# Optimization experiments

Hardware: AMD Instinct MI355X
Metric: run time of the kernel (lower is better)

## Reference

```python
import jax, jax.numpy as jnp
import numpy as np

DIM = 1024
HEADS = 16
HEAD_DIM = DIM // HEADS
SCALE = HEAD_DIM ** -0.5


def setup_inputs() -> dict:
    key = jax.random.key(0)
    k_x, k_qkv, k_ow, k_ob = jax.random.split(key, 4)
    B, N = 4, 2048
    x = jax.random.normal(k_x, (B, N, DIM), dtype=jnp.float32)
    # nn.Linear(dim, 3*dim, bias=False): weight [3*dim, dim]; we store transposed [dim, 3*dim]
    w_qkv = jax.random.normal(k_qkv, (DIM, 3 * DIM), dtype=jnp.float32) * (DIM ** -0.5)
    w_out = jax.random.normal(k_ow, (DIM, DIM), dtype=jnp.float32) * (DIM ** -0.5)
    b_out = jax.random.normal(k_ob, (DIM,), dtype=jnp.float32) * 0.01
    return {"x": x, "w_qkv": w_qkv, "w_out": w_out, "b_out": b_out}


def reference(x, w_qkv, w_out, b_out):
    B, N, D = x.shape
    H, hd = HEADS, HEAD_DIM
    qkv = x @ w_qkv                                  # [B, N, 3D]
    qkv = qkv.reshape(B, N, 3, H, hd).transpose(2, 0, 3, 1, 4)  # [3, B, H, N, hd]
    q, k, v = qkv[0], qkv[1], qkv[2]
    dots = jnp.einsum('bhnd,bhmd->bhnm', q, k) * SCALE  # [B, H, N, N]
    attn = jax.nn.softmax(dots, axis=-1)
    out = jnp.einsum('bhnm,bhmd->bhnd', attn, v)     # [B, H, N, hd]
    out = out.transpose(0, 2, 1, 3).reshape(B, N, D)
    return out @ w_out + b_out
```

## Files before the change

kernel.cpp:

```cpp
#include <hip/hip_runtime.h>
#include <hip/hip_bf16.h>

#define BSZ   4
#define NSEQ  2048
#define DIMM  1024
#define NHEAD 16
#define HD    64
#define N3    (3*DIMM)
#define MTOK  (BSZ*NSEQ)
#define SCALE 0.125f
#define CQ    0.18033688011112042f

typedef __attribute__((ext_vector_type(8))) short    short8;
typedef __attribute__((ext_vector_type(4))) short    short4v;
typedef __attribute__((ext_vector_type(2))) unsigned uint2v;
typedef __attribute__((ext_vector_type(8))) __bf16   bf16x8;
typedef __attribute__((ext_vector_type(4))) float    f32x4;

__device__ inline short f2bf(float f) {
    unsigned u = __builtin_bit_cast(unsigned, f);
    u += 0x7fffu + ((u >> 16) & 1u);
    return (short)(u >> 16);
}

__device__ inline unsigned pack_bf16(float a, float b) {
    unsigned ua = __builtin_bit_cast(unsigned, a) + 0x8000u;
    unsigned ub = __builtin_bit_cast(unsigned, b) + 0x8000u;
    return __builtin_amdgcn_perm(ub, ua, 0x07060302u);
}

__device__ inline float fast_exp2(float x) {
#if __has_builtin(__builtin_amdgcn_exp2f)
    return __builtin_amdgcn_exp2f(x);
#else
    return exp2f(x);
#endif
}

__device__ inline bf16x8 lds_frag(const short* p) {
    return __builtin_bit_cast(bf16x8, *(const short8*)p);
}

__device__ inline bf16x8 glb_frag(const short* p) {
    return __builtin_bit_cast(bf16x8, *(const short8*)p);
}

__device__ inline void gld_lds16(const short* g, short* l) {
    __builtin_amdgcn_global_load_lds(
        (const __attribute__((address_space(1))) void*)g,
        (__attribute__((address_space(3))) void*)l, 16, 0, 0);
}

__global__ __launch_bounds__(256)
void cvt_bf16(const float* __restrict__ src, short* __restrict__ dst, int n8)
{
    int i = blockIdx.x * 256 + threadIdx.x;
    if (i >= n8) return;
    float4 v0 = ((const float4*)src)[i * 2];
    float4 v1 = ((const float4*)src)[i * 2 + 1];
    short8 s = { f2bf(v0.x), f2bf(v0.y), f2bf(v0.z), f2bf(v0.w),
                 f2bf(v1.x), f2bf(v1.y), f2bf(v1.z), f2bf(v1.w) };
    ((short8*)dst)[i] = s;
}

__global__ __launch_bounds__(256)
void transpose_bf16(const float* __restrict__ src, short* __restrict__ dst,
                    int K, int N)
{
    __shared__ float tile[32][33];
    const int n0 = blockIdx.x * 32, k0 = blockIdx.y * 32;
    const int tx = threadIdx.x, ty = threadIdx.y;
    #pragma unroll
    for (int i = 0; i < 4; ++i)
        tile[ty + i * 8][tx] = src[(size_t)(k0 + ty + i * 8) * N + n0 + tx];
    __syncthreads();
    #pragma unroll
    for (int i = 0; i < 4; ++i)
        dst[(size_t)(n0 + ty + i * 8) * K + k0 + tx] = f2bf(tile[tx][ty + i * 8]);
}

#define GEMM_KLOOP(APTR, BPTR)                                                 \
    for (int k0 = 0; k0 < DIMM; k0 += 32) {                                    \
        _Pragma("unroll")                                                      \
        for (int j = 0; j < 2; ++j) {                                          \
            int c = j * 256 + tid;                                             \
            int r = c >> 2, jj = c & 3;                                        \
            int gc = jj ^ ((r >> 1) & 3);                                      \
            gld_lds16(APTR + (size_t)(row0 + r) * DIMM + k0 + gc * 8,          \
                      As + c * 8);                                             \
            gld_lds16(BPTR + (size_t)(col0 + r) * DIMM + k0 + gc * 8,         \
                      Bs + c * 8);                                             \
        }                                                                      \
        __syncthreads();                                                       \
        bf16x8 af[4], bfr[4];                                                  \
        _Pragma("unroll")                                                      \
        for (int mt = 0; mt < 4; ++mt) {                                       \
            int row = wm + mt * 16 + l16;                                      \
            af[mt] = lds_frag(&As[row * 32 + (quad ^ ((row >> 1) & 3)) * 8]);  \
        }                                                                      \
        _Pragma("unroll")                                                      \
        for (int nt = 0; nt < 4; ++nt) {                                       \
            int row = wn + nt * 16 + l16;                                      \
            bfr[nt] = lds_frag(&Bs[row * 32 + (quad ^ ((row >> 1) & 3)) * 8]); \
        }                                                                      \
        _Pragma("unroll")                                                      \
        for (int mt = 0; mt < 4; ++mt)                                         \
            _Pragma("unroll")                                                  \
            for (int nt = 0; nt < 4; ++nt)                                     \
                acc[mt][nt] = __builtin_amdgcn_mfma_f32_16x16x32_bf16(         \
                    af[mt], bfr[nt], acc[mt][nt], 0, 0, 0);                    \
        __syncthreads();                                                       \
    }

__global__ __launch_bounds__(256, 2)
void gemm_qkv(const short* __restrict__ a, const short* __restrict__ bt,
              short* __restrict__ qo, short* __restrict__ ko,
              short* __restrict__ vo)
{
    __shared__ short As[128 * 32];
    __shared__ short Bs[128 * 32];
    const int tid  = threadIdx.x;
    const int wave = tid >> 6, lane = tid & 63;
    const int quad = lane >> 4, l16 = lane & 15;
    const int row0 = blockIdx.x * 128, col0 = blockIdx.y * 128;
    const int wm = (wave >> 1) * 64, wn = (wave & 1) * 64;

    f32x4 acc[4][4] = {};
    GEMM_KLOOP(a, bt)

    #pragma unroll
    for (int mt = 0; mt < 4; ++mt) {
        #pragma unroll
        for (int nt = 0; nt < 4; ++nt) {
            int gcol  = col0 + wn + nt * 16 + l16;
            int which = gcol >> 10;
            int cc    = gcol & 1023;
            int h     = cc >> 6, d = cc & 63;
            int growb = row0 + wm + mt * 16 + quad * 4;
            int b_    = growb >> 11;
            int n_    = growb & 2047;
            int bh    = b_ * NHEAD + h;
            if (which == 2) {
                short4v s = { f2bf(acc[mt][nt][0]), f2bf(acc[mt][nt][1]),
                              f2bf(acc[mt][nt][2]), f2bf(acc[mt][nt][3]) };
                *(short4v*)(vo + ((size_t)bh * HD + d) * NSEQ + n_) = s;
            } else if (which == 0) {
                #pragma unroll
                for (int r = 0; r < 4; ++r)
                    qo[((size_t)bh * NSEQ + n_ + r) * HD + d] =
                        f2bf(acc[mt][nt][r] * CQ);
            } else {
                #pragma unroll
                for (int r = 0; r < 4; ++r)
                    ko[((size_t)bh * NSEQ + n_ + r) * HD + d] = f2bf(acc[mt][nt][r]);
            }
        }
    }
}

__global__ __launch_bounds__(256, 3)
void attn(const short* __restrict__ q, const short* __restrict__ k,
          const short* __restrict__ vt, short* __restrict__ o)
{
    __shared__ short Ks[2][64 * 64];
    __shared__ short Ps[4][32 * 72];

    const int tid  = threadIdx.x;
    const int wave = tid >> 6, lane = tid & 63;
    const int quad = lane >> 4, l16 = lane & 15;
    const int bh   = blockIdx.y;
    const int q0   = blockIdx.x * 128;
    const size_t qkbase = (size_t)bh * NSEQ * HD;
    const size_t vbase  = (size_t)bh * HD * NSEQ;

    bf16x8 qf[2][2];
    #pragma unroll
    for (int g = 0; g < 2; ++g)
        #pragma unroll
        for (int ks = 0; ks < 2; ++ks)
            qf[g][ks] = glb_frag(q + qkbase +
                (size_t)(q0 + wave * 32 + g * 16 + l16) * HD + ks * 32 + quad * 8);

    f32x4 oacc[4][2] = {};
    float lsum[2] = {0.f, 0.f};
    short* Pw = &Ps[wave][0];

    const int  sr   = tid >> 3, sj = tid & 7;
    const int  soff = sr * HD + ((sj ^ (sr & 7)) * 8);
    const short* kbh = k + qkbase;

    gld_lds16(kbh + soff,            &Ks[0][tid * 8]);
    gld_lds16(kbh + soff + 32 * HD,  &Ks[0][2048 + tid * 8]);

    for (int t = 0; t < NSEQ / 64; ++t) {
        const int kv0 = t * 64;
        __syncthreads();
        if (t + 1 < NSEQ / 64) {
            const short* src = kbh + (size_t)(kv0 + 64) * HD;
            short* dst = &Ks[(t + 1) & 1][0];
            gld_lds16(src + soff,           dst + tid * 8);
            gld_lds16(src + soff + 32 * HD, dst + 2048 + tid * 8);
        }
        const short* Kb = &Ks[t & 1][0];

        bf16x8 vf[2][4];
        #pragma unroll
        for (int ks2 = 0; ks2 < 2; ++ks2)
            #pragma unroll
            for (int ot = 0; ot < 4; ++ot)
                vf[ks2][ot] = glb_frag(vt + vbase +
                    (size_t)(ot * 16 + l16) * NSEQ + kv0 + ks2 * 32 + quad * 8);

        f32x4 sacc[4][2] = {};
        #pragma unroll
        for (int nt = 0; nt < 4; ++nt) {
            int row = nt * 16 + l16;
            #pragma unroll
            for (int ks = 0; ks < 2; ++ks) {
                bf16x8 kf = lds_frag(&Kb[row * 64 + (((ks * 4 + quad) ^ (row & 7)) * 8)]);
                #pragma unroll
                for (int g = 0; g < 2; ++g)
                    sacc[nt][g] = __builtin_amdgcn_mfma_f32_16x16x32_bf16(
                        kf, qf[g][ks], sacc[nt][g], 0, 0, 0);
            }
        }

        #pragma unroll
        for (int g = 0; g < 2; ++g) {
            #pragma unroll
            for (int nt = 0; nt < 4; ++nt) {
                float p0 = fast_exp2(sacc[nt][g][0]);
                float p1 = fast_exp2(sacc[nt][g][1]);
                float p2 = fast_exp2(sacc[nt][g][2]);
                float p3 = fast_exp2(sacc[nt][g][3]);
                lsum[g] += (p0 + p1) + (p2 + p3);
                uint2v u = { pack_bf16(p0, p1), pack_bf16(p2, p3) };
                *(uint2v*)&Pw[(g * 16 + l16) * 72 + nt * 16 + quad * 4] = u;
            }
        }

        #pragma unroll
        for (int ks2 = 0; ks2 < 2; ++ks2) {
            bf16x8 pf[2];
            #pragma unroll
            for (int g = 0; g < 2; ++g)
                pf[g] = lds_frag(&Pw[(g * 16 + l16) * 72 + ks2 * 32 + quad * 8]);
            #pragma unroll
            for (int ot = 0; ot < 4; ++ot)
                #pragma unroll
                for (int g = 0; g < 2; ++g)
                    oacc[ot][g] = __builtin_amdgcn_mfma_f32_16x16x32_bf16(
                        vf[ks2][ot], pf[g], oacc[ot][g], 0, 0, 0);
        }
    }

    const int b_ = bh >> 4, h = bh & 15;
    float inv[2];
    #pragma unroll
    for (int g = 0; g < 2; ++g) {
        float l = lsum[g];
        l += __shfl_xor(l, 16);
        l += __shfl_xor(l, 32);
        inv[g] = 1.f / l;
    }
    #pragma unroll
    for (int ot = 0; ot < 4; ++ot) {
        #pragma unroll
        for (int g = 0; g < 2; ++g) {
            short4v s4 = { f2bf(oacc[ot][g][0] * inv[g]),
                           f2bf(oacc[ot][g][1] * inv[g]),
                           f2bf(oacc[ot][g][2] * inv[g]),
                           f2bf(oacc[ot][g][3] * inv[g]) };
            *(short4v*)(o + ((size_t)b_ * NSEQ + q0 + wave * 32 + g * 16 + l16) * DIMM +
                        h * HD + ot * 16 + quad * 4) = s4;
        }
    }
}

__global__ __launch_bounds__(256, 3)
void gemm_out(const short* __restrict__ a, const short* __restrict__ bt,
              const float* __restrict__ bias, float* __restrict__ out)
{
    __shared__ short As[64 * 32];
    __shared__ short Bs[128 * 32];
    const int tid  = threadIdx.x;
    const int wave = tid >> 6, lane = tid & 63;
    const int quad = lane >> 4, l16 = lane & 15;
    const int row0 = blockIdx.x * 64, col0 = blockIdx.y * 128;
    const int wm = (wave & 1) * 32, wn = (wave >> 1) * 64;

    f32x4 acc[2][4] = {};

    for (int k0 = 0; k0 < DIMM; k0 += 32) {
        {
            int r = tid >> 2, jj = tid & 3;
            int gc = jj ^ ((r >> 1) & 3);
            gld_lds16(a + (size_t)(row0 + r) * DIMM + k0 + gc * 8, As + tid * 8);
        }
        #pragma unroll
        for (int j = 0; j < 2; ++j) {
            int c = j * 256 + tid;
            int r = c >> 2, jj = c & 3;
            int gc = jj ^ ((r >> 1) & 3);
            gld_lds16(bt + (size_t)(col0 + r) * DIMM + k0 + gc * 8, Bs + c * 8);
        }
        __syncthreads();
        bf16x8 af[2], bfr[4];
        #pragma unroll
        for (int mt = 0; mt < 2; ++mt) {
            int row = wm + mt * 16 + l16;
            af[mt] = lds_frag(&As[row * 32 + (quad ^ ((row >> 1) & 3)) * 8]);
        }
        #pragma unroll
        for (int nt = 0; nt < 4; ++nt) {
            int row = wn + nt * 16 + l16;
            bfr[nt] = lds_frag(&Bs[row * 32 + (quad ^ ((row >> 1) & 3)) * 8]);
        }
        #pragma unroll
        for (int mt = 0; mt < 2; ++mt)
            #pragma unroll
            for (int nt = 0; nt < 4; ++nt)
                acc[mt][nt] = __builtin_amdgcn_mfma_f32_16x16x32_bf16(
                    af[mt], bfr[nt], acc[mt][nt], 0, 0, 0);
        __syncthreads();
    }

    #pragma unroll
    for (int mt = 0; mt < 2; ++mt) {
        #pragma unroll
        for (int nt = 0; nt < 4; ++nt) {
            int gcol = col0 + wn + nt * 16 + l16;
            float bb = bias[gcol];
            #pragma unroll
            for (int r = 0; r < 4; ++r) {
                int grow = row0 + wm + mt * 16 + quad * 4 + r;
                out[(size_t)grow * DIMM + gcol] = acc[mt][nt][r] + bb;
            }
        }
    }
}

extern "C" void kernel_launch(void* const* d_in, const int* in_sizes, int n_in,
                              void* d_out, int out_size, void* d_ws, size_t ws_size,
                              hipStream_t stream)
{
    const float* x     = (const float*)d_in[0];
    const float* w_qkv = (const float*)d_in[1];
    const float* w_out = (const float*)d_in[2];
    const float* b_out = (const float*)d_in[3];
    float* out = (float*)d_out;

    const size_t per = (size_t)BSZ * NHEAD * NSEQ * HD;
    short* q     = (short*)d_ws;
    short* kk    = q  + per;
    short* v     = kk + per;
    short* xb_ob = v  + per;
    short* wqkvT = xb_ob + per;
    short* woutT = wqkvT + (size_t)N3 * DIMM;

    cvt_bf16<<<(int)(per / 8 / 256), 256, 0, stream>>>(x, xb_ob, (int)(per / 8));
    transpose_bf16<<<dim3(N3 / 32, DIMM / 32), dim3(32, 8), 0, stream>>>(w_qkv, wqkvT, DIMM, N3);
    transpose_bf16<<<dim3(DIMM / 32, DIMM / 32), dim3(32, 8), 0, stream>>>(w_out, woutT, DIMM, DIMM);

    gemm_qkv<<<dim3(MTOK / 128, N3 / 128), 256, 0, stream>>>(xb_ob, wqkvT, q, kk, v);
    attn<<<dim3(NSEQ / 128, BSZ * NHEAD), 256, 0, stream>>>(q, kk, v, xb_ob);
    gemm_out<<<dim3(MTOK / 64, DIMM / 128), 256, 0, stream>>>(xb_ob, woutT, b_out, out);
}
```

Baseline: 319.6 us.

## Fuse prep kernels and remap grids for XCD-aware L2 locality

Merges the x conversion and the two weight transposes into one prepass launch, which removes two kernel launches. Replaces the 2D grids of the QKV GEMM, attention and output GEMM with 1D grids. Block ids are remapped so that blocks landing on the same XCD (round-robin by id&7) share weight columns or the same head's K/V, aiming for better L2 reuse. The risk is a worse overall traversal order across XCDs and extra index arithmetic.

```diff
diff --git a/kernel.cpp b/kernel.cpp
--- a/kernel.cpp
+++ b/kernel.cpp
@@ -51,25 +51,13 @@
         (__attribute__((address_space(3))) void*)l, 16, 0, 0);
 }
 
-__global__ __launch_bounds__(256)
-void cvt_bf16(const float* __restrict__ src, short* __restrict__ dst, int n8)
-{
-    int i = blockIdx.x * 256 + threadIdx.x;
-    if (i >= n8) return;
-    float4 v0 = ((const float4*)src)[i * 2];
-    float4 v1 = ((const float4*)src)[i * 2 + 1];
-    short8 s = { f2bf(v0.x), f2bf(v0.y), f2bf(v0.z), f2bf(v0.w),
-                 f2bf(v1.x), f2bf(v1.y), f2bf(v1.z), f2bf(v1.w) };
-    ((short8*)dst)[i] = s;
-}
-
-__global__ __launch_bounds__(256)
-void transpose_bf16(const float* __restrict__ src, short* __restrict__ dst,
-                    int K, int N)
+__device__ inline void transpose_tile(const float* __restrict__ src,
+                                      short* __restrict__ dst,
+                                      int K, int N, int bx, int by, int tid)
 {
     __shared__ float tile[32][33];
-    const int n0 = blockIdx.x * 32, k0 = blockIdx.y * 32;
-    const int tx = threadIdx.x, ty = threadIdx.y;
+    const int n0 = bx * 32, k0 = by * 32;
+    const int tx = tid & 31, ty = tid >> 5;
     #pragma unroll
     for (int i = 0; i < 4; ++i)
         tile[ty + i * 8][tx] = src[(size_t)(k0 + ty + i * 8) * N + n0 + tx];
@@ -77,6 +65,28 @@
     #pragma unroll
     for (int i = 0; i < 4; ++i)
         dst[(size_t)(n0 + ty + i * 8) * K + k0 + tx] = f2bf(tile[tx][ty + i * 8]);
+}
+
+__global__ __launch_bounds__(256)
+void prepass(const float* __restrict__ x, short* __restrict__ xb,
+             const float* __restrict__ wqkv, short* __restrict__ wqkvT,
+             const float* __restrict__ wout, short* __restrict__ woutT)
+{
+    const int b = blockIdx.x, tid = threadIdx.x;
+    if (b < 4096) {
+        int i = b * 256 + tid;
+        float4 v0 = ((const float4*)x)[i * 2];
+        float4 v1 = ((const float4*)x)[i * 2 + 1];
+        short8 s = { f2bf(v0.x), f2bf(v0.y), f2bf(v0.z), f2bf(v0.w),
+                     f2bf(v1.x), f2bf(v1.y), f2bf(v1.z), f2bf(v1.w) };
+        ((short8*)xb)[i] = s;
+    } else if (b < 7168) {
+        int idx = b - 4096;
+        transpose_tile(wqkv, wqkvT, DIMM, N3, idx % 96, idx / 96, tid);
+    } else {
+        int idx = b - 7168;
+        transpose_tile(wout, woutT, DIMM, DIMM, idx & 31, idx >> 5, tid);
+    }
 }
 
 #define GEMM_KLOOP(APTR, BPTR)                                                 \
@@ -122,7 +132,11 @@
     const int tid  = threadIdx.x;
     const int wave = tid >> 6, lane = tid & 63;
     const int quad = lane >> 4, l16 = lane & 15;
-    const int row0 = blockIdx.x * 128, col0 = blockIdx.y * 128;
+    const int id   = blockIdx.x;
+    const int xcd  = id & 7, j = id >> 3;
+    const int jc   = j - (j / 3) * 3;
+    const int row0 = (j / 3) * 128;
+    const int col0 = (xcd * 3 + jc) * 128;
     const int wm = (wave >> 1) * 64, wn = (wave & 1) * 64;
 
     f32x4 acc[4][4] = {};
@@ -168,8 +182,10 @@
     const int tid  = threadIdx.x;
     const int wave = tid >> 6, lane = tid & 63;
     const int quad = lane >> 4, l16 = lane & 15;
-    const int bh   = blockIdx.y;
-    const int q0   = blockIdx.x * 128;
+    const int id   = blockIdx.x;
+    const int xcd  = id & 7, j = id >> 3;
+    const int bh   = xcd * 8 + (j >> 4);
+    const int q0   = (j & 15) * 128;
     const size_t qkbase = (size_t)bh * NSEQ * HD;
     const size_t vbase  = (size_t)bh * HD * NSEQ;
 
@@ -286,7 +302,8 @@
     const int tid  = threadIdx.x;
     const int wave = tid >> 6, lane = tid & 63;
     const int quad = lane >> 4, l16 = lane & 15;
-    const int row0 = blockIdx.x * 64, col0 = blockIdx.y * 128;
+    const int id   = blockIdx.x;
+    const int row0 = (id >> 3) * 64, col0 = (id & 7) * 128;
     const int wm = (wave & 1) * 32, wn = (wave >> 1) * 64;
 
     f32x4 acc[2][4] = {};
@@ -358,11 +375,8 @@
     short* wqkvT = xb_ob + per;
     short* woutT = wqkvT + (size_t)N3 * DIMM;
 
-    cvt_bf16<<<(int)(per / 8 / 256), 256, 0, stream>>>(x, xb_ob, (int)(per / 8));
-    transpose_bf16<<<dim3(N3 / 32, DIMM / 32), dim3(32, 8), 0, stream>>>(w_qkv, wqkvT, DIMM, N3);
-    transpose_bf16<<<dim3(DIMM / 32, DIMM / 32), dim3(32, 8), 0, stream>>>(w_out, woutT, DIMM, DIMM);
-
-    gemm_qkv<<<dim3(MTOK / 128, N3 / 128), 256, 0, stream>>>(xb_ob, wqkvT, q, kk, v);
-    attn<<<dim3(NSEQ / 128, BSZ * NHEAD), 256, 0, stream>>>(q, kk, v, xb_ob);
-    gemm_out<<<dim3(MTOK / 64, DIMM / 128), 256, 0, stream>>>(xb_ob, woutT, b_out, out);
-}
+    prepass<<<8192, 256, 0, stream>>>(x, xb_ob, w_qkv, wqkvT, w_out, woutT);
+    gemm_qkv<<<1536, 256, 0, stream>>>(xb_ob, wqkvT, q, kk, v);
+    attn<<<1024, 256, 0, stream>>>(q, kk, v, xb_ob);
+    gemm_out<<<1024, 256, 0, stream>>>(xb_ob, woutT, b_out, out);
+}
```

After: 320.1 us. No clear change (+0.1%).
